# Kernel tuning notes

Measured on AMD Instinct MI355X. Metric: run time of the kernel, lower is better.

The kernel has to match this reference:

```python
import jax, jax.numpy as jnp
import numpy as np

B, S, N, F = 4, 256, 128, 64
D = 128          # d_model == 2*F so encoder/decoder dims agree
NH = 4           # hard-coded num_heads in both MHA blocks


def _linear(x, w, b):
    # torch nn.Linear: y = x @ W.T + b, W: (out, in)
    return x @ w.T + b


def _mha(q, k, v, w_in, b_in, w_out, b_out, nh):
    # torch nn.MultiheadAttention (batch_first=True) with packed in_proj
    bq, sq, e = q.shape
    hd = e // nh
    qp = _linear(q, w_in[:e], b_in[:e])
    kp = _linear(k, w_in[e:2 * e], b_in[e:2 * e])
    vp = _linear(v, w_in[2 * e:], b_in[2 * e:])
    qh = qp.reshape(bq, sq, nh, hd)
    kh = kp.reshape(bq, k.shape[1], nh, hd)
    vh = vp.reshape(bq, v.shape[1], nh, hd)
    scores = jnp.einsum('bqhd,bkhd->bhqk', qh, kh) / np.sqrt(hd).astype(np.float32)
    attn = jax.nn.softmax(scores, axis=-1)
    out = jnp.einsum('bhqk,bkhd->bqhd', attn, vh).reshape(bq, sq, e)
    return _linear(out, w_out, b_out)


def _pos_enc(s, d):
    pos = jnp.arange(s, dtype=jnp.float32)[:, None]
    div = jnp.exp(jnp.arange(0, d, 2, dtype=jnp.float32) * (-np.log(10000.0) / d))
    pe = jnp.zeros((s, d), dtype=jnp.float32)
    pe = pe.at[:, 0::2].set(jnp.sin(pos * div))
    pe = pe.at[:, 1::2].set(jnp.cos(pos * div))
    return pe


def _haar_decouple(x):
    # exact vectorized pywt haar dwt + single-branch idwt (even seq_len)
    b, s, n, f = x.shape
    pairs = x.reshape(b, s // 2, 2, n, f)
    avg = (pairs[:, :, 0] + pairs[:, :, 1]) * 0.5  # idwt(cA, None) value
    dif = (pairs[:, :, 0] - pairs[:, :, 1]) * 0.5  # idwt(None, cD) value
    x_l = jnp.stack([avg, avg], axis=2).reshape(b, s, n, f)
    x_h = jnp.stack([dif, -dif], axis=2).reshape(b, s, n, f)
    return x_l, x_h


def setup_inputs() -> dict:
    key = jax.random.key(0)
    ks = jax.random.split(key, 32)
    p = lambda i, shp: jax.random.normal(ks[i], shp, jnp.float32) * 0.02
    return {
        'x': jax.random.normal(ks[0], (B, S, N, F), jnp.float32),
        'ts': jax.random.randint(ks[1], (B, S), 0, 252),
        'ta_w_in': p(2, (3 * D, D)), 'ta_b_in': p(3, (3 * D,)),
        'ta_w_out': p(4, (D, D)), 'ta_b_out': p(5, (D,)),
        'conv_w': p(6, (D, 2 * F, 3)), 'conv_b': p(7, (D,)),
        'pl_w': p(8, (D, D)), 'pl_b': p(9, (D,)),
        'ph_w': p(10, (D, D)), 'ph_b': p(11, (D,)),
        'as_w_in': p(12, (3 * D, D)), 'as_b_in': p(13, (3 * D,)),
        'as_w_out': p(14, (D, D)), 'as_b_out': p(15, (D,)),
        'ac_w_in': p(16, (3 * D, D)), 'ac_b_in': p(17, (3 * D,)),
        'ac_w_out': p(18, (D, D)), 'ac_b_out': p(19, (D,)),
        'rl_w': p(20, (1, D)), 'rl_b': p(21, (1,)),
        'cl_w': p(22, (2, D)), 'cl_b': p(23, (2,)),
        'rf_w': p(24, (1, D)), 'rf_b': p(25, (1,)),
        'cf_w': p(26, (2, D)), 'cf_b': p(27, (2,)),
    }


def reference(x, ts, ta_w_in, ta_b_in, ta_w_out, ta_b_out, conv_w, conv_b,
              pl_w, pl_b, ph_w, ph_b, as_w_in, as_b_in, as_w_out, as_b_out,
              ac_w_in, ac_b_in, ac_w_out, ac_b_out, rl_w, rl_b, cl_w, cl_b,
              rf_w, rf_b, cf_w, cf_b):
    b, s, n, f = x.shape
    # --- DecouplingFlowLayer (vectorized haar) ---
    x_l, x_h = _haar_decouple(x)
    xl_cat = jnp.concatenate([x, x_l], axis=-1)  # (b,s,n,2f)
    xh_cat = jnp.concatenate([x, x_h], axis=-1)
    e = 2 * f
    # --- DualFrequencyEncoder ---
    pe = _pos_enc(s, e)
    xl_flat = xl_cat.transpose(0, 2, 1, 3).reshape(b * n, s, e) + pe
    x_tatt = _mha(xl_flat, xl_flat, xl_flat, ta_w_in, ta_b_in, ta_w_out, ta_b_out, NH)
    x_l_gat = x_tatt.reshape(b, s, n, e)  # faithful raw .view() as in torch
    xh_flat = xh_cat.transpose(0, 2, 3, 1).reshape(b * n, e, s)
    conv = jax.lax.conv_general_dilated(
        xh_flat, conv_w, window_strides=(1,), padding=[(2, 2)],
        rhs_dilation=(2,), dimension_numbers=('NCH', 'OIH', 'NCH'))
    conv = jax.nn.relu(conv + conv_b[None, :, None])
    x_h_gat = conv.reshape(b, n, -1, s).transpose(0, 3, 1, 2)  # (b,s,n,D)
    d = x_h_gat.shape[-1]
    # ts -> time_embedding is computed then discarded in the original forward: dead code
    # --- DualFrequencyFusionDecoder ---
    y_l = x_l_gat.reshape(b * n, s, d)
    y_h = x_h_gat.reshape(b * n, s, d)
    q_l = _linear(y_l, pl_w, pl_b)
    k_h = _linear(y_h, ph_w, ph_b)
    y_l2 = _linear(q_l, pl_w, pl_b)  # predictor_l applied twice, as in torch
    lreg = _linear(y_l2, rl_w, rl_b).reshape(b, s, n)
    lcla = jax.nn.softmax(_linear(y_l2, cl_w, cl_b), axis=-1).reshape(b, s, n, 2)
    a_self = _mha(q_l, q_l, q_l, as_w_in, as_b_in, as_w_out, as_b_out, NH)
    a_cross = _mha(q_l, k_h, k_h, ac_w_in, ac_b_in, ac_w_out, ac_b_out, NH)
    fused = (a_self + a_cross).reshape(b, s, n, d)
    reg = _linear(fused, rf_w, rf_b)[..., 0]
    cla = jax.nn.softmax(_linear(fused, cf_w, cf_b), axis=-1)
    return reg, cla, lreg, lcla
```

## Files before the change

### kernel.cpp

```cpp
#include <hip/hip_runtime.h>
#include <hip/hip_bf16.h>

typedef __attribute__((ext_vector_type(8))) short short8v;
typedef __attribute__((ext_vector_type(4))) short short4v;
typedef __attribute__((ext_vector_type(4))) float f32x4;
typedef __hip_bfloat16 bh;

constexpr long SF_ELEMS = 131072L * 128;
#define MFMA16(a, b, c) __builtin_amdgcn_mfma_f32_16x16x32_bf16((a), (b), (c), 0, 0, 0)

__device__ __forceinline__ short bh_bits(float x) {
  bh h = __float2bfloat16(x);
  return *reinterpret_cast<short*>(&h);
}


__global__ __launch_bounds__(256) void sf_wcvt(const float* __restrict__ s0, const float* __restrict__ s1,
                                               const float* __restrict__ s2, const float* __restrict__ s3,
                                               const float* __restrict__ s4, const float* __restrict__ s5,
                                               const float* __restrict__ s6, const float* __restrict__ s7,
                                               const float* __restrict__ cw,
                                               bh* __restrict__ dst) {
  int i = blockIdx.x * 256 + threadIdx.x;
  float v;
  if      (i <  49152) v = s0[i];
  else if (i <  65536) v = s1[i - 49152];
  else if (i <  81920) v = s2[i - 65536];
  else if (i <  98304) v = s3[i - 81920];
  else if (i < 147456) v = s4[i - 98304];
  else if (i < 163840) v = s5[i - 147456];
  else if (i < 212992) v = s6[i - 163840];
  else if (i < 229376) v = s7[i - 212992];
  else if (i < 278528) {
    int j = i - 229376;
    int tap = j >> 14, rem = j & 16383;
    v = cw[rem * 3 + tap];
  } else return;
  dst[i] = __float2bfloat16(v);
}

__global__ __launch_bounds__(256) void sf_pe(float* __restrict__ pe) {
  int i = blockIdx.x * 256 + threadIdx.x;
  int e = i & 127, s = i >> 7;
  int ii = e >> 1;
  float dv = expf(-0.0719557945041855f * (float)(2 * ii));
  float ang = (float)s * dv;
  pe[i] = (e & 1) ? cosf(ang) : sinf(ang);
}

__global__ __launch_bounds__(256) void sf_buildzx(const float* __restrict__ x,
                                                  const float* __restrict__ pe,
                                                  bh* __restrict__ z,
                                                  bh* __restrict__ xh) {
  long i = (long)blockIdx.x * 256 + threadIdx.x;
  if (i >= SF_ELEMS) return;
  int e = (int)(i & 127);
  int s = (int)((i >> 7) & 255);
  int r = (int)(i >> 15);
  int b = r >> 7, stk = r & 127;
  float zv, hv;
  if (e < 64) {
    float val = x[(((long)b * 256 + s) * 128 + stk) * 64 + e];
    zv = val; hv = val;
  } else {
    int f = e - 64;
    int t2 = s >> 1;
    float a0 = x[(((long)b * 256 + 2 * t2) * 128 + stk) * 64 + f];
    float a1 = x[(((long)b * 256 + 2 * t2 + 1) * 128 + stk) * 64 + f];
    zv = 0.5f * (a0 + a1);
    float d = 0.5f * (a0 - a1);
    hv = (s & 1) ? -d : d;
  }
  z[i] = __float2bfloat16(zv + pe[s * 128 + e]);
  xh[i] = __float2bfloat16(hv);
}

__global__ __launch_bounds__(256) void sf_lin(const bh* __restrict__ X,
                                              const bh* __restrict__ Wb,
                                              const float* __restrict__ bias,
                                              bh* __restrict__ Y) {
  __shared__ bh Lw[4][32][140];
  const int t = threadIdx.x, lane = t & 63, w = t >> 6;
  const int lr = lane & 15, lg = lane >> 4;
  const long R0 = (long)blockIdx.x * 128 + w * 32;
  const f32x4 z4 = {0.f, 0.f, 0.f, 0.f};
  short8v a[2][4];
#pragma unroll
  for (int ks = 0; ks < 4; ++ks) {
    a[0][ks] = *reinterpret_cast<const short8v*>(X + (R0 + lr) * 128 + ks * 32 + lg * 8);
    a[1][ks] = *reinterpret_cast<const short8v*>(X + (R0 + 16 + lr) * 128 + ks * 32 + lg * 8);
  }
  f32x4 acc[2][8];
#pragma unroll
  for (int m = 0; m < 2; ++m)
#pragma unroll
    for (int n = 0; n < 8; ++n) acc[m][n] = z4;
#pragma unroll
  for (int ks = 0; ks < 4; ++ks) {
#pragma unroll
    for (int n = 0; n < 8; ++n) {
      short8v b = *reinterpret_cast<const short8v*>(Wb + (long)(n * 16 + lr) * 128 + ks * 32 + lg * 8);
      acc[0][n] = MFMA16(a[0][ks], b, acc[0][n]);
      acc[1][n] = MFMA16(a[1][ks], b, acc[1][n]);
    }
  }
#pragma unroll
  for (int n = 0; n < 8; ++n) {
    float bv = bias[n * 16 + lr];
#pragma unroll
    for (int m = 0; m < 2; ++m)
#pragma unroll
      for (int r = 0; r < 4; ++r)
        Lw[w][m * 16 + 4 * lg + r][n * 16 + lr] = __float2bfloat16(acc[m][n][r] + bv);
  }
#pragma unroll
  for (int c = 0; c < 8; ++c) {
    int row_l = c * 4 + lg;
    short8v v = *reinterpret_cast<const short8v*>(&Lw[w][row_l][lr * 8]);
    *reinterpret_cast<short8v*>(Y + (R0 + row_l) * 128 + lr * 8) = v;
  }
}

__global__ __launch_bounds__(256) void sf_convm(const bh* __restrict__ Xh,
                                                const bh* __restrict__ Wr,
                                                const float* __restrict__ bias,
                                                bh* __restrict__ Yh) {
  __shared__ bh Lw[4][32][140];
  const int t = threadIdx.x, lane = t & 63, w = t >> 6;
  const int lr = lane & 15, lg = lane >> 4;
  const int bnc = blockIdx.x >> 1;
  const int half = blockIdx.x & 1;
  const int b = bnc >> 7, stk = bnc & 127;
  const int R0 = half * 128 + w * 32;
  const f32x4 z4 = {0.f, 0.f, 0.f, 0.f};
  const short8v zf = {0, 0, 0, 0, 0, 0, 0, 0};
  f32x4 acc[2][8];
#pragma unroll
  for (int m = 0; m < 2; ++m)
#pragma unroll
    for (int n = 0; n < 8; ++n) acc[m][n] = z4;
#pragma unroll
  for (int tap = 0; tap < 3; ++tap) {
    const int shift = 2 * tap - 2;
#pragma unroll
    for (int ks = 0; ks < 4; ++ks) {
      int s0 = R0 + lr + shift;
      int s1 = s0 + 16;
      short8v a0 = zf, a1 = zf;
      if ((unsigned)s0 < 256u)
        a0 = *reinterpret_cast<const short8v*>(Xh + ((long)bnc * 256 + s0) * 128 + ks * 32 + lg * 8);
      if ((unsigned)s1 < 256u)
        a1 = *reinterpret_cast<const short8v*>(Xh + ((long)bnc * 256 + s1) * 128 + ks * 32 + lg * 8);
#pragma unroll
      for (int n = 0; n < 8; ++n) {
        short8v bb = *reinterpret_cast<const short8v*>(Wr + (long)tap * 16384 + (long)(n * 16 + lr) * 128 + ks * 32 + lg * 8);
        acc[0][n] = MFMA16(a0, bb, acc[0][n]);
        acc[1][n] = MFMA16(a1, bb, acc[1][n]);
      }
    }
  }
#pragma unroll
  for (int n = 0; n < 8; ++n) {
    float bv = bias[n * 16 + lr];
#pragma unroll
    for (int m = 0; m < 2; ++m)
#pragma unroll
      for (int r = 0; r < 4; ++r)
        Lw[w][m * 16 + 4 * lg + r][n * 16 + lr] = __float2bfloat16(fmaxf(acc[m][n][r] + bv, 0.f));
  }
#pragma unroll
  for (int c = 0; c < 8; ++c) {
    int row_l = c * 4 + lg;
    int sc = R0 + row_l;
    int rp = b * 128 + (sc >> 1);
    int sp = ((sc & 1) << 7) + stk;
    short8v v = *reinterpret_cast<const short8v*>(&Lw[w][row_l][lr * 8]);
    *reinterpret_cast<short8v*>(Yh + ((long)rp * 256 + sp) * 128 + lr * 8) = v;
  }
}

__global__ __launch_bounds__(256) void sf_attnp(const bh* Qsrc, const bh* KVsrc,
                                                const bh* __restrict__ Win,
                                                const float* __restrict__ bin,
                                                bh* __restrict__ O) {
  __shared__ bh Ks[256][36];
  __shared__ bh Vt[32][260];
  __shared__ bh QP[4][64][36];
  const int t = threadIdx.x, lane = t & 63, w = t >> 6;
  const int lr = lane & 15, lg = lane >> 4;
  const int bn = blockIdx.x >> 2, h = blockIdx.x & 3;
  const long R0 = (long)bn * 256;
  const int ch = h * 32;
  const f32x4 z4 = {0.f, 0.f, 0.f, 0.f};
  const float SC2 = 0.2550351f;
  {
    short8v wq[2][4];
#pragma unroll
    for (int n = 0; n < 2; ++n)
#pragma unroll
      for (int ks = 0; ks < 4; ++ks)
        wq[n][ks] = *reinterpret_cast<const short8v*>(Win + (long)(ch + n * 16 + lr) * 128 + ks * 32 + lg * 8);
#pragma unroll
    for (int m2 = 0; m2 < 4; ++m2) {
      short8v asv[4];
#pragma unroll
      for (int ks = 0; ks < 4; ++ks)
        asv[ks] = *reinterpret_cast<const short8v*>(Qsrc + (R0 + w * 64 + m2 * 16 + lr) * 128 + ks * 32 + lg * 8);
#pragma unroll
      for (int n = 0; n < 2; ++n) {
        f32x4 acc = z4;
#pragma unroll
        for (int ks = 0; ks < 4; ++ks) acc = MFMA16(asv[ks], wq[n][ks], acc);
        float bb = bin[ch + n * 16 + lr];
#pragma unroll
        for (int r = 0; r < 4; ++r)
          QP[w][m2 * 16 + 4 * lg + r][n * 16 + lr] = __float2bfloat16((acc[r] + bb) * SC2);
      }
    }
  }
  {
    short8v wk[2][4], wv[2][4];
#pragma unroll
    for (int n = 0; n < 2; ++n)
#pragma unroll
      for (int ks = 0; ks < 4; ++ks) {
        wk[n][ks] = *reinterpret_cast<const short8v*>(Win + (long)(128 + ch + n * 16 + lr) * 128 + ks * 32 + lg * 8);
        wv[n][ks] = *reinterpret_cast<const short8v*>(Win + (long)(256 + ch + n * 16 + lr) * 128 + ks * 32 + lg * 8);
      }
#pragma unroll
    for (int m2 = 0; m2 < 4; ++m2) {
      short8v asv[4];
#pragma unroll
      for (int ks = 0; ks < 4; ++ks)
        asv[ks] = *reinterpret_cast<const short8v*>(KVsrc + (R0 + w * 64 + m2 * 16 + lr) * 128 + ks * 32 + lg * 8);
#pragma unroll
      for (int n = 0; n < 2; ++n) {
        f32x4 ak = z4, av = z4;
#pragma unroll
        for (int ks = 0; ks < 4; ++ks) {
          ak = MFMA16(asv[ks], wk[n][ks], ak);
          av = MFMA16(asv[ks], wv[n][ks], av);
        }
        float bk = bin[128 + ch + n * 16 + lr];
        float bv = bin[256 + ch + n * 16 + lr];
#pragma unroll
        for (int r = 0; r < 4; ++r)
          Ks[w * 64 + m2 * 16 + 4 * lg + r][n * 16 + lr] = __float2bfloat16(ak[r] + bk);
        short4v pv;
#pragma unroll
        for (int r = 0; r < 4; ++r) pv[r] = bh_bits(av[r] + bv);
        *reinterpret_cast<short4v*>(&Vt[n * 16 + lr][w * 64 + m2 * 16 + 4 * lg]) = pv;
      }
    }
  }
  __syncthreads();
  short8v aq[4];
#pragma unroll
  for (int mt = 0; mt < 4; ++mt)
    aq[mt] = *reinterpret_cast<const short8v*>(&QP[w][mt * 16 + lr][lg * 8]);
  bh* plp = &QP[w][0][0];
  f32x4 Oacc[4][2];
  float psum[4] = {0.f, 0.f, 0.f, 0.f};
#pragma unroll
  for (int mt = 0; mt < 4; ++mt) { Oacc[mt][0] = z4; Oacc[mt][1] = z4; }
#pragma unroll
  for (int kt = 0; kt < 4; ++kt) {
    short8v bvf[2][2];
#pragma unroll
    for (int dt = 0; dt < 2; ++dt)
#pragma unroll
      for (int ks = 0; ks < 2; ++ks)
        bvf[dt][ks] = *reinterpret_cast<const short8v*>(&Vt[dt * 16 + lr][kt * 64 + ks * 32 + lg * 8]);
#pragma unroll
    for (int mt = 0; mt < 4; ++mt) {
      f32x4 st[4];
#pragma unroll
      for (int nt = 0; nt < 4; ++nt) {
        short8v bk = *reinterpret_cast<const short8v*>(&Ks[kt * 64 + nt * 16 + lr][lg * 8]);
        st[nt] = MFMA16(bk, aq[mt], z4);
      }
      float ps = 0.f;
#pragma unroll
      for (int nt = 0; nt < 4; ++nt) {
        float p0 = exp2f(st[nt][0]);
        float p1 = exp2f(st[nt][1]);
        float p2 = exp2f(st[nt][2]);
        float p3 = exp2f(st[nt][3]);
        ps += (p0 + p1) + (p2 + p3);
        short4v pk;
        pk[0] = bh_bits(p0); pk[1] = bh_bits(p1); pk[2] = bh_bits(p2); pk[3] = bh_bits(p3);
        *reinterpret_cast<short4v*>(&plp[lr * 72 + nt * 16 + 4 * lg]) = pk;
      }
      psum[mt] += ps;
#pragma unroll
      for (int ks = 0; ks < 2; ++ks) {
        short8v ap = *reinterpret_cast<const short8v*>(&plp[lr * 72 + ks * 32 + lg * 8]);
        Oacc[mt][0] = MFMA16(ap, bvf[0][ks], Oacc[mt][0]);
        Oacc[mt][1] = MFMA16(ap, bvf[1][ks], Oacc[mt][1]);
      }
    }
  }
#pragma unroll
  for (int mt = 0; mt < 4; ++mt) {
    float ps = psum[mt];
    ps += __shfl_xor(ps, 16, 64);
    ps += __shfl_xor(ps, 32, 64);
    float inv = 1.f / ps;
#pragma unroll
    for (int r = 0; r < 4; ++r) {
      float invr = __shfl(inv, 4 * lg + r, 64);
      long row = R0 + w * 64 + mt * 16 + 4 * lg + r;
      O[row * 128 + ch + lr]      = __float2bfloat16(Oacc[mt][0][r] * invr);
      O[row * 128 + ch + 16 + lr] = __float2bfloat16(Oacc[mt][1][r] * invr);
    }
  }
}

__global__ __launch_bounds__(256) void sf_encdec(const bh* __restrict__ X,
                                                 const bh* __restrict__ Wo, const float* __restrict__ bo,
                                                 const bh* __restrict__ Wpl, const float* __restrict__ bpl,
                                                 const float* __restrict__ rw, const float* __restrict__ rb,
                                                 const float* __restrict__ cw, const float* __restrict__ cb,
                                                 bh* __restrict__ Yq, float* __restrict__ out,
                                                 long off_reg, long off_cla) {
  __shared__ bh Lw[4][32][140];
  __shared__ float hw[3][128];
  const int t = threadIdx.x, lane = t & 63, w = t >> 6;
  const int lr = lane & 15, lg = lane >> 4;
  const long R0 = (long)blockIdx.x * 128 + w * 32;
  const f32x4 z4 = {0.f, 0.f, 0.f, 0.f};
  if (t < 128) { hw[0][t] = rw[t]; hw[1][t] = cw[t]; hw[2][t] = cw[128 + t]; }
  {
    short8v a[2][4];
#pragma unroll
    for (int ks = 0; ks < 4; ++ks) {
      a[0][ks] = *reinterpret_cast<const short8v*>(X + (R0 + lr) * 128 + ks * 32 + lg * 8);
      a[1][ks] = *reinterpret_cast<const short8v*>(X + (R0 + 16 + lr) * 128 + ks * 32 + lg * 8);
    }
    f32x4 acc[2][8];
#pragma unroll
    for (int m = 0; m < 2; ++m)
#pragma unroll
      for (int n = 0; n < 8; ++n) acc[m][n] = z4;
#pragma unroll
    for (int ks = 0; ks < 4; ++ks)
#pragma unroll
      for (int n = 0; n < 8; ++n) {
        short8v b = *reinterpret_cast<const short8v*>(Wo + (long)(n * 16 + lr) * 128 + ks * 32 + lg * 8);
        acc[0][n] = MFMA16(a[0][ks], b, acc[0][n]);
        acc[1][n] = MFMA16(a[1][ks], b, acc[1][n]);
      }
#pragma unroll
    for (int n = 0; n < 8; ++n) {
      float bv = bo[n * 16 + lr];
#pragma unroll
      for (int m = 0; m < 2; ++m)
#pragma unroll
        for (int r = 0; r < 4; ++r)
          Lw[w][m * 16 + 4 * lg + r][n * 16 + lr] = __float2bfloat16(acc[m][n][r] + bv);
    }
  }
#pragma unroll
  for (int stage = 0; stage < 2; ++stage) {
    short8v a[2][4];
#pragma unroll
    for (int ks = 0; ks < 4; ++ks) {
      a[0][ks] = *reinterpret_cast<const short8v*>(&Lw[w][lr][ks * 32 + lg * 8]);
      a[1][ks] = *reinterpret_cast<const short8v*>(&Lw[w][16 + lr][ks * 32 + lg * 8]);
    }
    f32x4 acc[2][8];
#pragma unroll
    for (int m = 0; m < 2; ++m)
#pragma unroll
      for (int n = 0; n < 8; ++n) acc[m][n] = z4;
#pragma unroll
    for (int ks = 0; ks < 4; ++ks)
#pragma unroll
      for (int n = 0; n < 8; ++n) {
        short8v b = *reinterpret_cast<const short8v*>(Wpl + (long)(n * 16 + lr) * 128 + ks * 32 + lg * 8);
        acc[0][n] = MFMA16(a[0][ks], b, acc[0][n]);
        acc[1][n] = MFMA16(a[1][ks], b, acc[1][n]);
      }
#pragma unroll
    for (int n = 0; n < 8; ++n) {
      float bv = bpl[n * 16 + lr];
#pragma unroll
      for (int m = 0; m < 2; ++m)
#pragma unroll
        for (int r = 0; r < 4; ++r)
          Lw[w][m * 16 + 4 * lg + r][n * 16 + lr] = __float2bfloat16(acc[m][n][r] + bv);
    }
    if (stage == 0) {
#pragma unroll
      for (int c = 0; c < 8; ++c) {
        int row_l = c * 4 + lg;
        short8v v = *reinterpret_cast<const short8v*>(&Lw[w][row_l][lr * 8]);
        *reinterpret_cast<short8v*>(Yq + (R0 + row_l) * 128 + lr * 8) = v;
      }
    }
  }
  __syncthreads();
  {
    const int rr = lane >> 1, hh = lane & 1;
    float d0 = 0.f, d1 = 0.f, d2 = 0.f;
#pragma unroll
    for (int j = 0; j < 8; ++j) {
      short8v v8 = *reinterpret_cast<const short8v*>(&Lw[w][rr][hh * 64 + j * 8]);
      const bh* vv = reinterpret_cast<const bh*>(&v8);
#pragma unroll
      for (int k = 0; k < 8; ++k) {
        float f = __bfloat162float(vv[k]);
        int c = hh * 64 + j * 8 + k;
        d0 = fmaf(f, hw[0][c], d0);
        d1 = fmaf(f, hw[1][c], d1);
        d2 = fmaf(f, hw[2][c], d2);
      }
    }
    d0 += __shfl_xor(d0, 1, 64);
    d1 += __shfl_xor(d1, 1, 64);
    d2 += __shfl_xor(d2, 1, 64);
    if (hh == 0) {
      long row = R0 + rr;
      d0 += rb[0]; d1 += cb[0]; d2 += cb[1];
      float mx = fmaxf(d1, d2);
      float e1 = __expf(d1 - mx), e2 = __expf(d2 - mx);
      float inv = 1.f / (e1 + e2);
      out[off_reg + row] = d0;
      out[off_cla + row * 2] = e1 * inv;
      out[off_cla + row * 2 + 1] = e2 * inv;
    }
  }
}

__global__ __launch_bounds__(256) void sf_fin(const bh* __restrict__ X,
                                              const bh* __restrict__ Was, const float* __restrict__ bo,
                                              const bh* __restrict__ Prev,
                                              const float* __restrict__ rw, const float* __restrict__ rb,
                                              const float* __restrict__ cw, const float* __restrict__ cb,
                                              float* __restrict__ out, long off_reg, long off_cla) {
  __shared__ bh Lw[4][32][140];
  __shared__ float hw[3][128];
  const int t = threadIdx.x, lane = t & 63, w = t >> 6;
  const int lr = lane & 15, lg = lane >> 4;
  const long R0 = (long)blockIdx.x * 128 + w * 32;
  const f32x4 z4 = {0.f, 0.f, 0.f, 0.f};
  if (t < 128) { hw[0][t] = rw[t]; hw[1][t] = cw[t]; hw[2][t] = cw[128 + t]; }
  {
    short8v a[2][4];
#pragma unroll
    for (int ks = 0; ks < 4; ++ks) {
      a[0][ks] = *reinterpret_cast<const short8v*>(X + (R0 + lr) * 128 + ks * 32 + lg * 8);
      a[1][ks] = *reinterpret_cast<const short8v*>(X + (R0 + 16 + lr) * 128 + ks * 32 + lg * 8);
    }
    f32x4 acc[2][8];
#pragma unroll
    for (int m = 0; m < 2; ++m)
#pragma unroll
      for (int n = 0; n < 8; ++n) acc[m][n] = z4;
#pragma unroll
    for (int ks = 0; ks < 4; ++ks)
#pragma unroll
      for (int n = 0; n < 8; ++n) {
        short8v b = *reinterpret_cast<const short8v*>(Was + (long)(n * 16 + lr) * 128 + ks * 32 + lg * 8);
        acc[0][n] = MFMA16(a[0][ks], b, acc[0][n]);
        acc[1][n] = MFMA16(a[1][ks], b, acc[1][n]);
      }
#pragma unroll
    for (int n = 0; n < 8; ++n) {
      float bv = bo[n * 16 + lr];
#pragma unroll
      for (int m = 0; m < 2; ++m)
#pragma unroll
        for (int r = 0; r < 4; ++r)
          Lw[w][m * 16 + 4 * lg + r][n * 16 + lr] = __float2bfloat16(acc[m][n][r] + bv);
    }
  }
  __syncthreads();
  {
    const int rr = lane >> 1, hh = lane & 1;
    float d0 = 0.f, d1 = 0.f, d2 = 0.f;
#pragma unroll
    for (int j = 0; j < 8; ++j) {
      short8v v8 = *reinterpret_cast<const short8v*>(&Lw[w][rr][hh * 64 + j * 8]);
      short8v p8 = *reinterpret_cast<const short8v*>(Prev + (R0 + rr) * 128 + hh * 64 + j * 8);
      const bh* vv = reinterpret_cast<const bh*>(&v8);
      const bh* pp = reinterpret_cast<const bh*>(&p8);
#pragma unroll
      for (int k = 0; k < 8; ++k) {
        float f = __bfloat162float(vv[k]) + __bfloat162float(pp[k]);
        int c = hh * 64 + j * 8 + k;
        d0 = fmaf(f, hw[0][c], d0);
        d1 = fmaf(f, hw[1][c], d1);
        d2 = fmaf(f, hw[2][c], d2);
      }
    }
    d0 += __shfl_xor(d0, 1, 64);
    d1 += __shfl_xor(d1, 1, 64);
    d2 += __shfl_xor(d2, 1, 64);
    if (hh == 0) {
      long row = R0 + rr;
      d0 += rb[0]; d1 += cb[0]; d2 += cb[1];
      float mx = fmaxf(d1, d2);
      float e1 = __expf(d1 - mx), e2 = __expf(d2 - mx);
      float inv = 1.f / (e1 + e2);
      out[off_reg + row] = d0;
      out[off_cla + row * 2] = e1 * inv;
      out[off_cla + row * 2 + 1] = e2 * inv;
    }
  }
}

extern "C" void kernel_launch(void* const* d_in, const int* in_sizes, int n_in,
                              void* d_out, int out_size, void* d_ws, size_t ws_size,
                              hipStream_t stream) {
  (void)in_sizes; (void)n_in; (void)out_size; (void)ws_size;
  const float* x       = (const float*)d_in[0];
  const float* ta_w_in = (const float*)d_in[2];
  const float* ta_b_in = (const float*)d_in[3];
  const float* ta_w_o  = (const float*)d_in[4];
  const float* ta_b_o  = (const float*)d_in[5];
  const float* conv_w  = (const float*)d_in[6];
  const float* conv_b  = (const float*)d_in[7];
  const float* pl_w    = (const float*)d_in[8];
  const float* pl_b    = (const float*)d_in[9];
  const float* ph_w    = (const float*)d_in[10];
  const float* ph_b    = (const float*)d_in[11];
  const float* as_w_in = (const float*)d_in[12];
  const float* as_b_in = (const float*)d_in[13];
  const float* as_w_o  = (const float*)d_in[14];
  const float* as_b_o  = (const float*)d_in[15];
  const float* ac_w_in = (const float*)d_in[16];
  const float* ac_b_in = (const float*)d_in[17];
  const float* ac_w_o  = (const float*)d_in[18];
  const float* ac_b_o  = (const float*)d_in[19];
  const float* rl_w    = (const float*)d_in[20];
  const float* rl_b    = (const float*)d_in[21];
  const float* cl_w    = (const float*)d_in[22];
  const float* cl_b    = (const float*)d_in[23];
  const float* rf_w    = (const float*)d_in[24];
  const float* rf_b    = (const float*)d_in[25];
  const float* cf_w    = (const float*)d_in[26];
  const float* cf_b    = (const float*)d_in[27];
  float* out = (float*)d_out;

  bh* S0 = (bh*)d_ws;
  bh* S1 = S0 + SF_ELEMS;
  bh* S2 = S1 + SF_ELEMS;
  bh* S3 = S2 + SF_ELEMS;
  bh* S4 = S3 + SF_ELEMS;
  bh* A  = S4 + SF_ELEMS;
  float* PE = (float*)(A + 278528);

  dim3 blk(256);
  const int GZ = (int)(SF_ELEMS / 256);
  const int GL = 1024;

  sf_wcvt<<<1088, blk, 0, stream>>>(ta_w_in, ta_w_o, pl_w, ph_w, ac_w_in, ac_w_o,
                                    as_w_in, as_w_o, conv_w, A);
  sf_pe<<<128, blk, 0, stream>>>(PE);

  sf_buildzx<<<GZ, blk, 0, stream>>>(x, PE, S0, S3);
  sf_attnp<<<2048, blk, 0, stream>>>(S0, S0, A, ta_b_in, S1);
  sf_encdec<<<GL, blk, 0, stream>>>(S1, A + 49152, ta_b_o, A + 65536, pl_b,
                                    rl_w, rl_b, cl_w, cl_b, S2, out,
                                    393216L, 524288L);
  sf_convm<<<1024, blk, 0, stream>>>(S3, A + 229376, conv_b, S4);
  sf_lin<<<GL, blk, 0, stream>>>(S4, A + 81920, ph_b, S0);

  sf_attnp<<<2048, blk, 0, stream>>>(S2, S0, A + 98304, ac_b_in, S3);
  sf_lin<<<GL, blk, 0, stream>>>(S3, A + 147456, ac_b_o, S4);

  sf_attnp<<<2048, blk, 0, stream>>>(S2, S2, A + 163840, as_b_in, S1);
  sf_fin<<<GL, blk, 0, stream>>>(S1, A + 212992, as_b_o, S4,
                                 rf_w, rf_b, cf_w, cf_b, out, 0L, 131072L);
}
```

Before: 471.2 us.

## Fuse conv with predictor_h linear and merge both attention out-projections into final head

The dilated conv kernel now applies the predictor_h linear to its ReLU output held in shared memory, so the separate linear pass that re-read the intermediate from global memory goes away. The final kernel now computes both the self- and cross-attention output projections, accumulating them into one MFMA accumulator with summed biases, then applies the regression and classifier heads. This drops two kernel launches and several full-tensor global round trips. In exchange the fused kernels need more registers, and the sum is accumulated in fp32 before the bf16 round, which changes rounding slightly.

```diff
diff --git a/kernel.cpp b/kernel.cpp
--- a/kernel.cpp
+++ b/kernel.cpp
@@ -75,110 +75,6 @@
   xh[i] = __float2bfloat16(hv);
 }
 
-__global__ __launch_bounds__(256) void sf_lin(const bh* __restrict__ X,
-                                              const bh* __restrict__ Wb,
-                                              const float* __restrict__ bias,
-                                              bh* __restrict__ Y) {
-  __shared__ bh Lw[4][32][140];
-  const int t = threadIdx.x, lane = t & 63, w = t >> 6;
-  const int lr = lane & 15, lg = lane >> 4;
-  const long R0 = (long)blockIdx.x * 128 + w * 32;
-  const f32x4 z4 = {0.f, 0.f, 0.f, 0.f};
-  short8v a[2][4];
-#pragma unroll
-  for (int ks = 0; ks < 4; ++ks) {
-    a[0][ks] = *reinterpret_cast<const short8v*>(X + (R0 + lr) * 128 + ks * 32 + lg * 8);
-    a[1][ks] = *reinterpret_cast<const short8v*>(X + (R0 + 16 + lr) * 128 + ks * 32 + lg * 8);
-  }
-  f32x4 acc[2][8];
-#pragma unroll
-  for (int m = 0; m < 2; ++m)
-#pragma unroll
-    for (int n = 0; n < 8; ++n) acc[m][n] = z4;
-#pragma unroll
-  for (int ks = 0; ks < 4; ++ks) {
-#pragma unroll
-    for (int n = 0; n < 8; ++n) {
-      short8v b = *reinterpret_cast<const short8v*>(Wb + (long)(n * 16 + lr) * 128 + ks * 32 + lg * 8);
-      acc[0][n] = MFMA16(a[0][ks], b, acc[0][n]);
-      acc[1][n] = MFMA16(a[1][ks], b, acc[1][n]);
-    }
-  }
-#pragma unroll
-  for (int n = 0; n < 8; ++n) {
-    float bv = bias[n * 16 + lr];
-#pragma unroll
-    for (int m = 0; m < 2; ++m)
-#pragma unroll
-      for (int r = 0; r < 4; ++r)
-        Lw[w][m * 16 + 4 * lg + r][n * 16 + lr] = __float2bfloat16(acc[m][n][r] + bv);
-  }
-#pragma unroll
-  for (int c = 0; c < 8; ++c) {
-    int row_l = c * 4 + lg;
-    short8v v = *reinterpret_cast<const short8v*>(&Lw[w][row_l][lr * 8]);
-    *reinterpret_cast<short8v*>(Y + (R0 + row_l) * 128 + lr * 8) = v;
-  }
-}
-
-__global__ __launch_bounds__(256) void sf_convm(const bh* __restrict__ Xh,
-                                                const bh* __restrict__ Wr,
-                                                const float* __restrict__ bias,
-                                                bh* __restrict__ Yh) {
-  __shared__ bh Lw[4][32][140];
-  const int t = threadIdx.x, lane = t & 63, w = t >> 6;
-  const int lr = lane & 15, lg = lane >> 4;
-  const int bnc = blockIdx.x >> 1;
-  const int half = blockIdx.x & 1;
-  const int b = bnc >> 7, stk = bnc & 127;
-  const int R0 = half * 128 + w * 32;
-  const f32x4 z4 = {0.f, 0.f, 0.f, 0.f};
-  const short8v zf = {0, 0, 0, 0, 0, 0, 0, 0};
-  f32x4 acc[2][8];
-#pragma unroll
-  for (int m = 0; m < 2; ++m)
-#pragma unroll
-    for (int n = 0; n < 8; ++n) acc[m][n] = z4;
-#pragma unroll
-  for (int tap = 0; tap < 3; ++tap) {
-    const int shift = 2 * tap - 2;
-#pragma unroll
-    for (int ks = 0; ks < 4; ++ks) {
-      int s0 = R0 + lr + shift;
-      int s1 = s0 + 16;
-      short8v a0 = zf, a1 = zf;
-      if ((unsigned)s0 < 256u)
-        a0 = *reinterpret_cast<const short8v*>(Xh + ((long)bnc * 256 + s0) * 128 + ks * 32 + lg * 8);
-      if ((unsigned)s1 < 256u)
-        a1 = *reinterpret_cast<const short8v*>(Xh + ((long)bnc * 256 + s1) * 128 + ks * 32 + lg * 8);
-#pragma unroll
-      for (int n = 0; n < 8; ++n) {
-        short8v bb = *reinterpret_cast<const short8v*>(Wr + (long)tap * 16384 + (long)(n * 16 + lr) * 128 + ks * 32 + lg * 8);
-        acc[0][n] = MFMA16(a0, bb, acc[0][n]);
-        acc[1][n] = MFMA16(a1, bb, acc[1][n]);
-      }
-    }
-  }
-#pragma unroll
-  for (int n = 0; n < 8; ++n) {
-    float bv = bias[n * 16 + lr];
-#pragma unroll
-    for (int m = 0; m < 2; ++m)
-#pragma unroll
-      for (int r = 0; r < 4; ++r)
-        Lw[w][m * 16 + 4 * lg + r][n * 16 + lr] = __float2bfloat16(fmaxf(acc[m][n][r] + bv, 0.f));
-  }
-#pragma unroll
-  for (int c = 0; c < 8; ++c) {
-    int row_l = c * 4 + lg;
-    int sc = R0 + row_l;
-    int rp = b * 128 + (sc >> 1);
-    int sp = ((sc & 1) << 7) + stk;
-    short8v v = *reinterpret_cast<const short8v*>(&Lw[w][row_l][lr * 8]);
-    *reinterpret_cast<short8v*>(Yh + ((long)rp * 256 + sp) * 128 + lr * 8) = v;
-  }
-}
-
 __global__ __launch_bounds__(256) void sf_attnp(const bh* Qsrc, const bh* KVsrc,
                                                 const bh* __restrict__ Win,
                                                 const float* __restrict__ bin,
@@ -316,6 +212,96 @@
   }
 }
 
+__global__ __launch_bounds__(256) void sf_convkh(const bh* __restrict__ Xh,
+                                                 const bh* __restrict__ Wr,
+                                                 const float* __restrict__ cbias,
+                                                 const bh* __restrict__ Wph,
+                                                 const float* __restrict__ bph,
+                                                 bh* __restrict__ KH) {
+  __shared__ bh Lw[4][32][140];
+  const int t = threadIdx.x, lane = t & 63, w = t >> 6;
+  const int lr = lane & 15, lg = lane >> 4;
+  const int bnc = blockIdx.x >> 1;
+  const int half = blockIdx.x & 1;
+  const int b = bnc >> 7, stk = bnc & 127;
+  const int R0 = half * 128 + w * 32;
+  const f32x4 z4 = {0.f, 0.f, 0.f, 0.f};
+  const short8v zf = {0, 0, 0, 0, 0, 0, 0, 0};
+  f32x4 acc[2][8];
+#pragma unroll
+  for (int m = 0; m < 2; ++m)
+#pragma unroll
+    for (int n = 0; n < 8; ++n) acc[m][n] = z4;
+#pragma unroll
+  for (int tap = 0; tap < 3; ++tap) {
+    const int shift = 2 * tap - 2;
+#pragma unroll
+    for (int ks = 0; ks < 4; ++ks) {
+      int s0 = R0 + lr + shift;
+      int s1 = s0 + 16;
+      short8v a0 = zf, a1 = zf;
+      if ((unsigned)s0 < 256u)
+        a0 = *reinterpret_cast<const short8v*>(Xh + ((long)bnc * 256 + s0) * 128 + ks * 32 + lg * 8);
+      if ((unsigned)s1 < 256u)
+        a1 = *reinterpret_cast<const short8v*>(Xh + ((long)bnc * 256 + s1) * 128 + ks * 32 + lg * 8);
+#pragma unroll
+      for (int n = 0; n < 8; ++n) {
+        short8v bb = *reinterpret_cast<const short8v*>(Wr + (long)tap * 16384 + (long)(n * 16 + lr) * 128 + ks * 32 + lg * 8);
+        acc[0][n] = MFMA16(a0, bb, acc[0][n]);
+        acc[1][n] = MFMA16(a1, bb, acc[1][n]);
+      }
+    }
+  }
+#pragma unroll
+  for (int n = 0; n < 8; ++n) {
+    float bv = cbias[n * 16 + lr];
+#pragma unroll
+    for (int m = 0; m < 2; ++m)
+#pragma unroll
+      for (int r = 0; r < 4; ++r)
+        Lw[w][m * 16 + 4 * lg + r][n * 16 + lr] = __float2bfloat16(fmaxf(acc[m][n][r] + bv, 0.f));
+  }
+  {
+    short8v a2[2][4];
+#pragma unroll
+    for (int ks = 0; ks < 4; ++ks) {
+      a2[0][ks] = *reinterpret_cast<const short8v*>(&Lw[w][lr][ks * 32 + lg * 8]);
+      a2[1][ks] = *reinterpret_cast<const short8v*>(&Lw[w][16 + lr][ks * 32 + lg * 8]);
+    }
+    f32x4 ac2[2][8];
+#pragma unroll
+    for (int m = 0; m < 2; ++m)
+#pragma unroll
+      for (int n = 0; n < 8; ++n) ac2[m][n] = z4;
+#pragma unroll
+    for (int ks = 0; ks < 4; ++ks)
+#pragma unroll
+      for (int n = 0; n < 8; ++n) {
+        short8v b2 = *reinterpret_cast<const short8v*>(Wph + (long)(n * 16 + lr) * 128 + ks * 32 + lg * 8);
+        ac2[0][n] = MFMA16(a2[0][ks], b2, ac2[0][n]);
+        ac2[1][n] = MFMA16(a2[1][ks], b2, ac2[1][n]);
+      }
+#pragma unroll
+    for (int n = 0; n < 8; ++n) {
+      float bv = bph[n * 16 + lr];
+#pragma unroll
+      for (int m = 0; m < 2; ++m)
+#pragma unroll
+        for (int r = 0; r < 4; ++r)
+          Lw[w][m * 16 + 4 * lg + r][n * 16 + lr] = __float2bfloat16(ac2[m][n][r] + bv);
+    }
+  }
+#pragma unroll
+  for (int c = 0; c < 8; ++c) {
+    int row_l = c * 4 + lg;
+    int sc = R0 + row_l;
+    int rp = b * 128 + (sc >> 1);
+    int sp = ((sc & 1) << 7) + stk;
+    short8v v = *reinterpret_cast<const short8v*>(&Lw[w][row_l][lr * 8]);
+    *reinterpret_cast<short8v*>(KH + ((long)rp * 256 + sp) * 128 + lr * 8) = v;
+  }
+}
+
 __global__ __launch_bounds__(256) void sf_encdec(const bh* __restrict__ X,
                                                  const bh* __restrict__ Wo, const float* __restrict__ bo,
                                                  const bh* __restrict__ Wpl, const float* __restrict__ bpl,
@@ -432,12 +418,13 @@
   }
 }
 
-__global__ __launch_bounds__(256) void sf_fin(const bh* __restrict__ X,
-                                              const bh* __restrict__ Was, const float* __restrict__ bo,
-                                              const bh* __restrict__ Prev,
-                                              const float* __restrict__ rw, const float* __restrict__ rb,
-                                              const float* __restrict__ cw, const float* __restrict__ cb,
-                                              float* __restrict__ out, long off_reg, long off_cla) {
+__global__ __launch_bounds__(256) void sf_fin2(const bh* __restrict__ Xs,
+                                               const bh* __restrict__ Was, const float* __restrict__ bs,
+                                               const bh* __restrict__ Xc,
+                                               const bh* __restrict__ Wac, const float* __restrict__ bc,
+                                               const float* __restrict__ rw, const float* __restrict__ rb,
+                                               const float* __restrict__ cw, const float* __restrict__ cb,
+                                               float* __restrict__ out, long off_reg, long off_cla) {
   __shared__ bh Lw[4][32][140];
   __shared__ float hw[3][128];
   const int t = threadIdx.x, lane = t & 63, w = t >> 6;
@@ -446,28 +433,46 @@
   const f32x4 z4 = {0.f, 0.f, 0.f, 0.f};
   if (t < 128) { hw[0][t] = rw[t]; hw[1][t] = cw[t]; hw[2][t] = cw[128 + t]; }
   {
-    short8v a[2][4];
-#pragma unroll
-    for (int ks = 0; ks < 4; ++ks) {
-      a[0][ks] = *reinterpret_cast<const short8v*>(X + (R0 + lr) * 128 + ks * 32 + lg * 8);
-      a[1][ks] = *reinterpret_cast<const short8v*>(X + (R0 + 16 + lr) * 128 + ks * 32 + lg * 8);
-    }
     f32x4 acc[2][8];
 #pragma unroll
     for (int m = 0; m < 2; ++m)
 #pragma unroll
       for (int n = 0; n < 8; ++n) acc[m][n] = z4;
-#pragma unroll
-    for (int ks = 0; ks < 4; ++ks)
-#pragma unroll
-      for (int n = 0; n < 8; ++n) {
-        short8v b = *reinterpret_cast<const short8v*>(Was + (long)(n * 16 + lr) * 128 + ks * 32 + lg * 8);
-        acc[0][n] = MFMA16(a[0][ks], b, acc[0][n]);
-        acc[1][n] = MFMA16(a[1][ks], b, acc[1][n]);
-      }
+    {
+      short8v a[2][4];
+#pragma unroll
+      for (int ks = 0; ks < 4; ++ks) {
+        a[0][ks] = *reinterpret_cast<const short8v*>(Xs + (R0 + lr) * 128 + ks * 32 + lg * 8);
+        a[1][ks] = *reinterpret_cast<const short8v*>(Xs + (R0 + 16 + lr) * 128 + ks * 32 + lg * 8);
+      }
+#pragma unroll
+      for (int ks = 0; ks < 4; ++ks)
+#pragma unroll
+        for (int n = 0; n < 8; ++n) {
+          short8v b = *reinterpret_cast<const short8v*>(Was + (long)(n * 16 + lr) * 128 + ks * 32 + lg * 8);
+          acc[0][n] = MFMA16(a[0][ks], b, acc[0][n]);
+          acc[1][n] = MFMA16(a[1][ks], b, acc[1][n]);
+        }
+    }
+    {
+      short8v a[2][4];
+#pragma unroll
+      for (int ks = 0; ks < 4; ++ks) {
+        a[0][ks] = *reinterpret_cast<const short8v*>(Xc + (R0 + lr) * 128 + ks * 32 + lg * 8);
+        a[1][ks] = *reinterpret_cast<const short8v*>(Xc + (R0 + 16 + lr) * 128 + ks * 32 + lg * 8);
+      }
+#pragma unroll
+      for (int ks = 0; ks < 4; ++ks)
+#pragma unroll
+        for (int n = 0; n < 8; ++n) {
+          short8v b = *reinterpret_cast<const short8v*>(Wac + (long)(n * 16 + lr) * 128 + ks * 32 + lg * 8);
+          acc[0][n] = MFMA16(a[0][ks], b, acc[0][n]);
+          acc[1][n] = MFMA16(a[1][ks], b, acc[1][n]);
+        }
+    }
 #pragma unroll
     for (int n = 0; n < 8; ++n) {
-      float bv = bo[n * 16 + lr];
+      float bv = bs[n * 16 + lr] + bc[n * 16 + lr];
 #pragma unroll
       for (int m = 0; m < 2; ++m)
 #pragma unroll
@@ -482,12 +487,10 @@
 #pragma unroll
     for (int j = 0; j < 8; ++j) {
       short8v v8 = *reinterpret_cast<const short8v*>(&Lw[w][rr][hh * 64 + j * 8]);
-      short8v p8 = *reinterpret_cast<const short8v*>(Prev + (R0 + rr) * 128 + hh * 64 + j * 8);
       const bh* vv = reinterpret_cast<const bh*>(&v8);
-      const bh* pp = reinterpret_cast<const bh*>(&p8);
 #pragma unroll
       for (int k = 0; k < 8; ++k) {
-        float f = __bfloat162float(vv[k]) + __bfloat162float(pp[k]);
+        float f = __bfloat162float(vv[k]);
         int c = hh * 64 + j * 8 + k;
         d0 = fmaf(f, hw[0][c], d0);
         d1 = fmaf(f, hw[1][c], d1);
@@ -564,13 +567,12 @@
   sf_encdec<<<GL, blk, 0, stream>>>(S1, A + 49152, ta_b_o, A + 65536, pl_b,
                                     rl_w, rl_b, cl_w, cl_b, S2, out,
                                     393216L, 524288L);
-  sf_convm<<<1024, blk, 0, stream>>>(S3, A + 229376, conv_b, S4);
-  sf_lin<<<GL, blk, 0, stream>>>(S4, A + 81920, ph_b, S0);
+  sf_convkh<<<1024, blk, 0, stream>>>(S3, A + 229376, conv_b, A + 81920, ph_b, S0);
 
   sf_attnp<<<2048, blk, 0, stream>>>(S2, S0, A + 98304, ac_b_in, S3);
-  sf_lin<<<GL, blk, 0, stream>>>(S3, A + 147456, ac_b_o, S4);
 
   sf_attnp<<<2048, blk, 0, stream>>>(S2, S2, A + 163840, as_b_in, S1);
-  sf_fin<<<GL, blk, 0, stream>>>(S1, A + 212992, as_b_o, S4,
-                                 rf_w, rf_b, cf_w, cf_b, out, 0L, 131072L);
-}
+
+  sf_fin2<<<GL, blk, 0, stream>>>(S1, A + 212992, as_b_o, S3, A + 147456, ac_b_o,
+                                  rf_w, rf_b, cf_w, cf_b, out, 0L, 131072L);
+}
```

After: 455.7 us. 1.03x faster.
